# Optimization experiments

Measured on AMD Instinct MI355X. Metric: run time of the kernel, lower is better.

The kernel has to match this reference:

```python
import jax, jax.numpy as jnp
import numpy as np

N_NODES = 100000
N_EDGES = 3200000
F_IN = 256
HEADS = 8
C_OUT = 8
NEG_SLOPE = 0.2


def setup_inputs() -> dict:
    key = jax.random.key(0)
    k1, k2, k3, k4, k5, k6 = jax.random.split(key, 6)
    x = jax.random.normal(k1, (N_NODES, F_IN), dtype=jnp.float32)
    edge_index = jax.random.randint(k2, (2, N_EDGES), 0, N_NODES, dtype=jnp.int64)
    W = jax.random.normal(k3, (F_IN, HEADS * C_OUT), dtype=jnp.float32) * (1.0 / np.sqrt(F_IN))
    att_src = jax.random.normal(k4, (HEADS, C_OUT), dtype=jnp.float32) * 0.1
    att_dst = jax.random.normal(k5, (HEADS, C_OUT), dtype=jnp.float32) * 0.1
    bias = jax.random.normal(k6, (HEADS * C_OUT,), dtype=jnp.float32) * 0.01
    return {"x": x, "edge_index": edge_index, "W": W, "att_src": att_src, "att_dst": att_dst, "bias": bias}


def reference(x, edge_index, W, att_src, att_dst, bias):
    # GATConv (PyG semantics), concat=True, inference (dropout off).
    N = x.shape[0]
    H, C = att_src.shape
    h = (x @ W).reshape(N, H, C)                      # [N,H,C] transformed features
    a_src = jnp.einsum('nhc,hc->nh', h, att_src)      # [N,H]
    a_dst = jnp.einsum('nhc,hc->nh', h, att_dst)      # [N,H]
    src, dst = edge_index[0], edge_index[1]
    # per-edge raw attention logits
    e = jax.nn.leaky_relu(a_src[src] + a_dst[dst], NEG_SLOPE)  # [E,H]
    # segment softmax over incoming edges of each destination node
    m = jax.ops.segment_max(e, dst, num_segments=N)            # [N,H]
    e = jnp.exp(e - m[dst])
    s = jax.ops.segment_sum(e, dst, num_segments=N)            # [N,H]
    alpha = e / (s[dst] + 1e-16)                               # [E,H]
    # scatter-add weighted neighbor features
    out = jax.ops.segment_sum(alpha[:, :, None] * h[src], dst, num_segments=N)  # [N,H,C]
    return out.reshape(N, H * C) + bias
```

## Files before the change

kernel.cpp:

```cpp
#include <hip/hip_runtime.h>
#include <hip/hip_fp16.h>
#include <math.h>

#define F_IN 256
#define HC 64
#define NHEAD 8
#define NEG 0.2f
#define BSH 7
#define BSZ 128
#define CAP 5376

__global__ __launch_bounds__(256) void k_gemm(
    const float* __restrict__ x, const float* __restrict__ W,
    const float* __restrict__ att_src, const float* __restrict__ att_dst,
    __half2* __restrict__ h2, float* __restrict__ asrc, float* __restrict__ adst, int N) {
  __shared__ float Wl[128 * HC];
  int t = threadIdx.x;
  int g = t >> 4, q = t & 15;
  int c0 = q * 4, hd = q >> 1, cb = c0 & 7;
  float as0 = att_src[hd * 8 + cb + 0], as1 = att_src[hd * 8 + cb + 1];
  float as2 = att_src[hd * 8 + cb + 2], as3 = att_src[hd * 8 + cb + 3];
  float ad0 = att_dst[hd * 8 + cb + 0], ad1 = att_dst[hd * 8 + cb + 1];
  float ad2 = att_dst[hd * 8 + cb + 2], ad3 = att_dst[hd * 8 + cb + 3];

  int nb = blockIdx.x * 128 + g * 8;
  const float* xr[8];
#pragma unroll
  for (int i = 0; i < 8; i++) {
    int id = nb + i;
    if (id > N - 1) id = N - 1;
    xr[i] = x + (size_t)id * F_IN;
  }
  float4 acc[8];
#pragma unroll
  for (int i = 0; i < 8; i++) acc[i] = make_float4(0.f, 0.f, 0.f, 0.f);

  for (int half = 0; half < 2; half++) {
    __syncthreads();
    for (int i = t * 4; i < 128 * HC; i += 1024)
      *(float4*)&Wl[i] = *(const float4*)&W[half * 128 * HC + i];
    __syncthreads();
    int kb = half * 128;
    for (int k = 0; k < 128; k += 4) {
      float4 w0 = *(float4*)&Wl[(k + 0) * HC + c0];
      float4 w1 = *(float4*)&Wl[(k + 1) * HC + c0];
      float4 w2 = *(float4*)&Wl[(k + 2) * HC + c0];
      float4 w3 = *(float4*)&Wl[(k + 3) * HC + c0];
#pragma unroll
      for (int i = 0; i < 8; i++) {
        float4 xv = *(const float4*)(xr[i] + kb + k);
        acc[i].x = fmaf(xv.x, w0.x, fmaf(xv.y, w1.x, fmaf(xv.z, w2.x, fmaf(xv.w, w3.x, acc[i].x))));
        acc[i].y = fmaf(xv.x, w0.y, fmaf(xv.y, w1.y, fmaf(xv.z, w2.y, fmaf(xv.w, w3.y, acc[i].y))));
        acc[i].z = fmaf(xv.x, w0.z, fmaf(xv.y, w1.z, fmaf(xv.z, w2.z, fmaf(xv.w, w3.z, acc[i].z))));
        acc[i].w = fmaf(xv.x, w0.w, fmaf(xv.y, w1.w, fmaf(xv.z, w2.w, fmaf(xv.w, w3.w, acc[i].w))));
      }
    }
  }

#pragma unroll
  for (int i = 0; i < 8; i++) {
    float ps = acc[i].x * as0 + acc[i].y * as1 + acc[i].z * as2 + acc[i].w * as3;
    float pd = acc[i].x * ad0 + acc[i].y * ad1 + acc[i].z * ad2 + acc[i].w * ad3;
    ps += __shfl_xor(ps, 1);
    pd += __shfl_xor(pd, 1);
    int id = nb + i;
    if (id < N) {
      union { uint2 u; __half2 p[2]; } pk;
      pk.p[0] = __halves2half2(__float2half_rn(acc[i].x), __float2half_rn(acc[i].y));
      pk.p[1] = __halves2half2(__float2half_rn(acc[i].z), __float2half_rn(acc[i].w));
      *(uint2*)(h2 + (size_t)id * 32 + (c0 >> 1)) = pk.u;
      if (!(q & 1)) {
        asrc[id * NHEAD + hd] = ps;
        adst[id * NHEAD + hd] = pd;
      }
    }
  }
}

__global__ void k_zero(int* __restrict__ p, int n) {
  int i = blockIdx.x * 256 + threadIdx.x;
  if (i < n) p[i] = 0;
}

__global__ __launch_bounds__(512) void k_partition(
    const int* __restrict__ edge, int* __restrict__ bcursor,
    unsigned int* __restrict__ entries, int E, int NB) {
  __shared__ unsigned long long srt8[8192];
  __shared__ int hist[1024];
  __shared__ int loff[1024];
  __shared__ int basearr[1024];
  __shared__ int pr[512];
  int t = threadIdx.x;
  int base = blockIdx.x * 8192;
  int cblk = min(8192, E - base);
  for (int i = t; i < 1024; i += 512) hist[i] = 0;
  __syncthreads();
#pragma unroll
  for (int j = 0; j < 16; j++) {
    int e = base + j * 512 + t;
    if (e < E) atomicAdd(&hist[edge[E + e] >> BSH], 1);
  }
  __syncthreads();
  int a = hist[2 * t], b = hist[2 * t + 1];
  pr[t] = a + b;
  __syncthreads();
  for (int off = 1; off < 512; off <<= 1) {
    int add = (t >= off) ? pr[t - off] : 0;
    __syncthreads();
    pr[t] += add;
    __syncthreads();
  }
  int excl = pr[t] - (a + b);
  loff[2 * t] = excl;
  loff[2 * t + 1] = excl + a;
  if (a > 0 && 2 * t < NB) basearr[2 * t] = atomicAdd(&bcursor[2 * t], a);
  if (b > 0 && 2 * t + 1 < NB) basearr[2 * t + 1] = atomicAdd(&bcursor[2 * t + 1], b);
  hist[2 * t] = excl;
  hist[2 * t + 1] = excl + a;
  __syncthreads();
#pragma unroll
  for (int j = 0; j < 16; j++) {
    int e = base + j * 512 + t;
    if (e < E) {
      int s = edge[e], d = edge[E + e];
      int p = atomicAdd(&hist[d >> BSH], 1);
      srt8[p] = ((unsigned long long)(unsigned int)d << 32) | (unsigned int)s;
    }
  }
  __syncthreads();
  for (int i = t; i < cblk; i += 512) {
    unsigned long long v = srt8[i];
    int d = (int)(v >> 32), s = (int)(v & 0xFFFFFFFFu);
    int bk = d >> BSH;
    int local = basearr[bk] + (i - loff[bk]);
    if (local < CAP)
      entries[(size_t)bk * CAP + local] = ((unsigned int)(d & (BSZ - 1)) << 17) | (unsigned int)s;
  }
}

__global__ __launch_bounds__(512, 6) void k_bagg(
    const unsigned int* __restrict__ entries, const int* __restrict__ bcursor,
    const __half2* __restrict__ h2, const float* __restrict__ asrc,
    const float* __restrict__ adst, const float* __restrict__ bias,
    float* __restrict__ out, int N) {
  __shared__ int srt[CAP];
  __shared__ int hist[BSZ];
  __shared__ int cur[BSZ];
  __shared__ int off[BSZ + 1];
  __shared__ int tmp[BSZ];
  int t = threadIdx.x;
  int bkt = blockIdx.x;
  int n0 = bkt << BSH;
  int ncnt = min(BSZ, N - n0);
  int cnt = bcursor[bkt];
  if (cnt > CAP) cnt = CAP;
  const unsigned int* ebase = entries + (size_t)bkt * CAP;
  for (int i = t; i < BSZ; i += 512) hist[i] = 0;
  __syncthreads();
  for (int i = t; i < cnt; i += 512)
    atomicAdd(&hist[ebase[i] >> 17], 1);
  __syncthreads();
  if (t < BSZ) tmp[t] = hist[t];
  __syncthreads();
  for (int o = 1; o < BSZ; o <<= 1) {
    int add = (t < BSZ && t >= o) ? tmp[t - o] : 0;
    __syncthreads();
    if (t < BSZ) tmp[t] += add;
    __syncthreads();
  }
  if (t < BSZ) { off[t] = tmp[t] - hist[t]; cur[t] = tmp[t] - hist[t]; }
  if (t == 0) off[BSZ] = cnt;
  __syncthreads();
  for (int i = t; i < cnt; i += 512) {
    unsigned int v = ebase[i];
    int p = atomicAdd(&cur[v >> 17], 1);
    srt[p] = (int)(v & 0x1FFFF);
  }
  __syncthreads();
  int wv = t >> 6, lane = t & 63;
  int sub = lane >> 5, sl = lane & 31;
  int head = sl >> 2;
  for (int nd = wv; nd < ncnt; nd += 8) {
    int node = n0 + nd;
    int sbeg = off[nd], send = off[nd + 1];
    float ad = adst[node * NHEAD + head];
    float ax = 0.f, ay = 0.f, wsum = 0.f;
    int k = sbeg + sub;
    for (; k + 6 < send; k += 8) {
      int s0 = srt[k];
      int s1 = srt[k + 2];
      int s2 = srt[k + 4];
      int s3 = srt[k + 6];
      float l0 = asrc[s0 * NHEAD + head] + ad;
      float l1 = asrc[s1 * NHEAD + head] + ad;
      float l2 = asrc[s2 * NHEAD + head] + ad;
      float l3 = asrc[s3 * NHEAD + head] + ad;
      __half2 v0 = h2[(size_t)s0 * 32 + sl];
      __half2 v1 = h2[(size_t)s1 * 32 + sl];
      __half2 v2 = h2[(size_t)s2 * 32 + sl];
      __half2 v3 = h2[(size_t)s3 * 32 + sl];
      float w0 = __expf(fmaxf(l0, NEG * l0));
      float w1 = __expf(fmaxf(l1, NEG * l1));
      float w2 = __expf(fmaxf(l2, NEG * l2));
      float w3 = __expf(fmaxf(l3, NEG * l3));
      float2 f0 = __half22float2(v0);
      float2 f1 = __half22float2(v1);
      float2 f2 = __half22float2(v2);
      float2 f3 = __half22float2(v3);
      ax = fmaf(w0, f0.x, fmaf(w1, f1.x, fmaf(w2, f2.x, fmaf(w3, f3.x, ax))));
      ay = fmaf(w0, f0.y, fmaf(w1, f1.y, fmaf(w2, f2.y, fmaf(w3, f3.y, ay))));
      wsum += (w0 + w1) + (w2 + w3);
    }
    for (; k < send; k += 2) {
      int s = srt[k];
      float lg = asrc[s * NHEAD + head] + ad;
      float w = __expf(fmaxf(lg, NEG * lg));
      float2 f = __half22float2(h2[(size_t)s * 32 + sl]);
      ax = fmaf(w, f.x, ax);
      ay = fmaf(w, f.y, ay);
      wsum += w;
    }
    ax += __shfl_xor(ax, 32);
    ay += __shfl_xor(ay, 32);
    wsum += __shfl_xor(wsum, 32);
    if (sub == 0) {
      float inv = wsum > 0.f ? 1.0f / wsum : 0.f;
      float2 bx = *(const float2*)&bias[2 * sl];
      float2 r;
      r.x = fmaf(ax, inv, bx.x);
      r.y = fmaf(ay, inv, bx.y);
      *(float2*)&out[(size_t)node * HC + 2 * sl] = r;
    }
  }
}

extern "C" void kernel_launch(void* const* d_in, const int* in_sizes, int n_in,
                              void* d_out, int out_size, void* d_ws, size_t ws_size,
                              hipStream_t stream) {
  const float* x = (const float*)d_in[0];
  const int* edge = (const int*)d_in[1];
  const float* W = (const float*)d_in[2];
  const float* att_src = (const float*)d_in[3];
  const float* att_dst = (const float*)d_in[4];
  const float* bias = (const float*)d_in[5];
  int N = in_sizes[0] / F_IN;
  int E = in_sizes[1] / 2;
  float* out = (float*)d_out;
  int NB = (N + BSZ - 1) >> BSH;

  __half2* h2 = (__half2*)d_ws;
  float* asrc = (float*)(h2 + (size_t)N * 32);
  float* adst = asrc + (size_t)N * NHEAD;
  int* bcursor = (int*)(adst + (size_t)N * NHEAD);
  unsigned int* entries = (unsigned int*)(bcursor + NB);

  int nch = (E + 8191) / 8192;

  k_zero<<<(NB + 255) / 256, 256, 0, stream>>>(bcursor, NB);
  k_gemm<<<(N + 127) / 128, 256, 0, stream>>>(x, W, att_src, att_dst, h2, asrc, adst, N);
  k_partition<<<nch, 512, 0, stream>>>(edge, bcursor, entries, E, NB);
  k_bagg<<<NB, 512, 0, stream>>>(entries, bcursor, h2, asrc, adst, bias, out, N);
}
```

Measured before the change: 369.2 us.

## Drop shared-memory W staging in GEMM, prefetch from global with smaller row tiles

The projection GEMM stops staging W into LDS with block-wide barriers and instead reads W directly from global memory (L1/L2 cached), using register double-buffering to prefetch the next k-slice of x and W. Rows per thread drop from 8 to 4 and the grid doubles, which raises occupancy and lowers register pressure. The aim is to remove LDS fill and barrier stalls and to hide global load latency. In exchange, each W element is reused across fewer rows, so there is more global/L1 traffic for W.

```diff
diff --git a/kernel.cpp b/kernel.cpp
--- a/kernel.cpp
+++ b/kernel.cpp
@@ -14,7 +14,6 @@
     const float* __restrict__ x, const float* __restrict__ W,
     const float* __restrict__ att_src, const float* __restrict__ att_dst,
     __half2* __restrict__ h2, float* __restrict__ asrc, float* __restrict__ adst, int N) {
-  __shared__ float Wl[128 * HC];
   int t = threadIdx.x;
   int g = t >> 4, q = t & 15;
   int c0 = q * 4, hd = q >> 1, cb = c0 & 7;
@@ -23,42 +22,48 @@
   float ad0 = att_dst[hd * 8 + cb + 0], ad1 = att_dst[hd * 8 + cb + 1];
   float ad2 = att_dst[hd * 8 + cb + 2], ad3 = att_dst[hd * 8 + cb + 3];
 
-  int nb = blockIdx.x * 128 + g * 8;
-  const float* xr[8];
-#pragma unroll
-  for (int i = 0; i < 8; i++) {
+  int nb = blockIdx.x * 64 + g * 4;
+  const float* xr[4];
+#pragma unroll
+  for (int i = 0; i < 4; i++) {
     int id = nb + i;
     if (id > N - 1) id = N - 1;
     xr[i] = x + (size_t)id * F_IN;
   }
-  float4 acc[8];
-#pragma unroll
-  for (int i = 0; i < 8; i++) acc[i] = make_float4(0.f, 0.f, 0.f, 0.f);
-
-  for (int half = 0; half < 2; half++) {
-    __syncthreads();
-    for (int i = t * 4; i < 128 * HC; i += 1024)
-      *(float4*)&Wl[i] = *(const float4*)&W[half * 128 * HC + i];
-    __syncthreads();
-    int kb = half * 128;
-    for (int k = 0; k < 128; k += 4) {
-      float4 w0 = *(float4*)&Wl[(k + 0) * HC + c0];
-      float4 w1 = *(float4*)&Wl[(k + 1) * HC + c0];
-      float4 w2 = *(float4*)&Wl[(k + 2) * HC + c0];
-      float4 w3 = *(float4*)&Wl[(k + 3) * HC + c0];
-#pragma unroll
-      for (int i = 0; i < 8; i++) {
-        float4 xv = *(const float4*)(xr[i] + kb + k);
-        acc[i].x = fmaf(xv.x, w0.x, fmaf(xv.y, w1.x, fmaf(xv.z, w2.x, fmaf(xv.w, w3.x, acc[i].x))));
-        acc[i].y = fmaf(xv.x, w0.y, fmaf(xv.y, w1.y, fmaf(xv.z, w2.y, fmaf(xv.w, w3.y, acc[i].y))));
-        acc[i].z = fmaf(xv.x, w0.z, fmaf(xv.y, w1.z, fmaf(xv.z, w2.z, fmaf(xv.w, w3.z, acc[i].z))));
-        acc[i].w = fmaf(xv.x, w0.w, fmaf(xv.y, w1.w, fmaf(xv.z, w2.w, fmaf(xv.w, w3.w, acc[i].w))));
-      }
-    }
-  }
-
-#pragma unroll
-  for (int i = 0; i < 8; i++) {
+  float4 acc[4];
+#pragma unroll
+  for (int i = 0; i < 4; i++) acc[i] = make_float4(0.f, 0.f, 0.f, 0.f);
+
+  const float* wp = W + c0;
+  float4 xv[4], wv[4], nxv[4], nwv[4];
+#pragma unroll
+  for (int i = 0; i < 4; i++) xv[i] = *(const float4*)(xr[i]);
+#pragma unroll
+  for (int j = 0; j < 4; j++) wv[j] = *(const float4*)(wp + j * HC);
+
+  for (int k = 0; k < F_IN; k += 4) {
+    int k2 = k + 4;
+    if (k2 < F_IN) {
+#pragma unroll
+      for (int i = 0; i < 4; i++) nxv[i] = *(const float4*)(xr[i] + k2);
+#pragma unroll
+      for (int j = 0; j < 4; j++) nwv[j] = *(const float4*)(wp + (size_t)(k2 + j) * HC);
+    }
+#pragma unroll
+    for (int i = 0; i < 4; i++) {
+      acc[i].x = fmaf(xv[i].x, wv[0].x, fmaf(xv[i].y, wv[1].x, fmaf(xv[i].z, wv[2].x, fmaf(xv[i].w, wv[3].x, acc[i].x))));
+      acc[i].y = fmaf(xv[i].x, wv[0].y, fmaf(xv[i].y, wv[1].y, fmaf(xv[i].z, wv[2].y, fmaf(xv[i].w, wv[3].y, acc[i].y))));
+      acc[i].z = fmaf(xv[i].x, wv[0].z, fmaf(xv[i].y, wv[1].z, fmaf(xv[i].z, wv[2].z, fmaf(xv[i].w, wv[3].z, acc[i].z))));
+      acc[i].w = fmaf(xv[i].x, wv[0].w, fmaf(xv[i].y, wv[1].w, fmaf(xv[i].z, wv[2].w, fmaf(xv[i].w, wv[3].w, acc[i].w))));
+    }
+#pragma unroll
+    for (int i = 0; i < 4; i++) xv[i] = nxv[i];
+#pragma unroll
+    for (int j = 0; j < 4; j++) wv[j] = nwv[j];
+  }
+
+#pragma unroll
+  for (int i = 0; i < 4; i++) {
     float ps = acc[i].x * as0 + acc[i].y * as1 + acc[i].z * as2 + acc[i].w * as3;
     float pd = acc[i].x * ad0 + acc[i].y * ad1 + acc[i].z * ad2 + acc[i].w * ad3;
     ps += __shfl_xor(ps, 1);
@@ -257,7 +262,7 @@
   int nch = (E + 8191) / 8192;
 
   k_zero<<<(NB + 255) / 256, 256, 0, stream>>>(bcursor, NB);
-  k_gemm<<<(N + 127) / 128, 256, 0, stream>>>(x, W, att_src, att_dst, h2, asrc, adst, N);
+  k_gemm<<<(N + 63) / 64, 256, 0, stream>>>(x, W, att_src, att_dst, h2, asrc, adst, N);
   k_partition<<<nch, 512, 0, stream>>>(edge, bcursor, entries, E, NB);
   k_bagg<<<NB, 512, 0, stream>>>(entries, bcursor, h2, asrc, adst, bias, out, N);
 }
```

After: 406.7 us. 1.1x slower.
